# Performance work log

Hardware: AMD Instinct MI355X
Metric: run time of the kernel (lower is better)

## Reference

```python
import jax, jax.numpy as jnp
import numpy as np

B, T, F, H = 256, 128, 1024, 512  # batch, input_size (time window), feature_dim, hidden_size


def setup_inputs() -> dict:
    key = jax.random.key(0)
    ks = jax.random.split(key, 7)
    in1 = T + 2 * H
    return {
        "h": jax.random.normal(ks[0], (B, H), dtype=jnp.float32),
        "s": jax.random.normal(ks[1], (B, H), dtype=jnp.float32),
        "x": jax.random.normal(ks[2], (B, T, F), dtype=jnp.float32),
        "W1": jax.random.normal(ks[3], (T, in1), dtype=jnp.float32) / np.sqrt(in1),
        "b1": jnp.zeros((T,), dtype=jnp.float32),
        "W2": jax.random.normal(ks[4], (1, T), dtype=jnp.float32) / np.sqrt(T),
        "b2": jnp.zeros((1,), dtype=jnp.float32),
    }


def reference(h, s, x, W1, b1, W2, b2):
    feature_dim = x.shape[-1]
    xp = jnp.transpose(x, (2, 0, 1))                     # [F, B, T]
    hb = jnp.broadcast_to(h[None], (feature_dim,) + h.shape)  # [F, B, H]
    sb = jnp.broadcast_to(s[None], (feature_dim,) + s.shape)  # [F, B, H]
    cat = jnp.concatenate([xp, hb, sb], axis=-1)         # [F, B, T+2H]
    u = jnp.einsum('fbk,tk->fbt', cat, W1) + b1          # [F, B, T]
    e = jnp.einsum('fbt,ot->fbo', jnp.tanh(u), W2) + b2  # [F, B, 1]
    alpha = jax.nn.softmax(e, axis=0)[..., 0]            # softmax over feature dim -> [F, B]
    return alpha.T                                       # [B, F]
```

## Files before the change

kernel.cpp:

```cpp
#include <hip/hip_runtime.h>
#include <hip/hip_bf16.h>


#define B_N 256
#define T_N 128
#define F_N 1024
#define H_N 512
#define IN1 1152

typedef __bf16 bf16x8 __attribute__((ext_vector_type(8)));
typedef float f32x16 __attribute__((ext_vector_type(16)));
typedef float f32x4_t __attribute__((ext_vector_type(4)));

__device__ __forceinline__ float wave_reduce_sum(float v) {
#pragma unroll
  for (int off = 32; off >= 1; off >>= 1) v += __shfl_xor(v, off, 64);
  return v;
}
__device__ __forceinline__ float wave_reduce_max(float v) {
#pragma unroll
  for (int off = 32; off >= 1; off >>= 1) v = fmaxf(v, __shfl_xor(v, off, 64));
  return v;
}

__global__ __launch_bounds__(1024) void kA_c(const float* __restrict__ h,
                                             const float* __restrict__ s,
                                             const float* __restrict__ W1,
                                             const float* __restrict__ b1,
                                             float* __restrict__ c) {
  int tid = threadIdx.x;
  int lane = tid & 63, wid = tid >> 6;
  int tg = blockIdx.x >> 6;
  int bg = blockIdx.x & 63;
  int t = tg * 4 + (wid >> 2);
  int b = bg * 4 + (wid & 3);
  const float4* wrow = reinterpret_cast<const float4*>(W1 + t * IN1 + T_N);
  const float4* hrow = reinterpret_cast<const float4*>(h + b * H_N);
  const float4* srow = reinterpret_cast<const float4*>(s + b * H_N);
  float acc = 0.f;
#pragma unroll
  for (int i = 0; i < 4; ++i) {
    int j4 = i * 64 + lane;
    float4 w = wrow[j4];
    float4 v = (i < 2) ? hrow[j4] : srow[j4 - 128];
    acc += w.x * v.x + w.y * v.y + w.z * v.z + w.w * v.w;
  }
  acc = wave_reduce_sum(acc);
  if (lane == 0) c[b * T_N + t] = acc + b1[t];
}

__global__ __launch_bounds__(256) void kA_frag(const float* __restrict__ W1,
                                               unsigned short* __restrict__ w1frag) {
  int i = blockIdx.x * 256 + threadIdx.x;
  int p0 = i * 2;
  int j = p0 & 7;
  int lane = (p0 >> 3) & 63;
  int kk = (p0 >> 9) & 7;
  int tt = (p0 >> 12) & 3;
  int t = tt * 32 + (lane & 31);
  int k = kk * 16 + 8 * (lane >> 5) + j;
  const float2 w = *reinterpret_cast<const float2*>(W1 + t * IN1 + k);
  __bf16 a = (__bf16)w.x, bq = (__bf16)w.y;
  unsigned short ua = __builtin_bit_cast(unsigned short, a);
  unsigned short ub = __builtin_bit_cast(unsigned short, bq);
  *reinterpret_cast<unsigned*>(w1frag + p0) = (unsigned)ua | ((unsigned)ub << 16);
}

__global__ __launch_bounds__(256) void kB_e(const float* __restrict__ x,
                                            const unsigned short* __restrict__ w1frag,
                                            const float* __restrict__ c,
                                            const float* __restrict__ W2,
                                            const float* __restrict__ b2,
                                            float* __restrict__ e) {
  __shared__ __align__(16) unsigned short w1lds[16384];
  __shared__ __align__(16) float clds[T_N];
  __shared__ __align__(16) float w2lds[T_N];
  int tid = threadIdx.x;
  int b = blockIdx.x >> 3;
  int fg = blockIdx.x & 7;

  {
    const uint4* src = reinterpret_cast<const uint4*>(w1frag);
    uint4* dst = reinterpret_cast<uint4*>(w1lds);
#pragma unroll
    for (int i = 0; i < 8; ++i) dst[tid + 256 * i] = src[tid + 256 * i];
  }
  if (tid < T_N) clds[tid] = c[b * T_N + tid];
  else if (tid < 2 * T_N) w2lds[tid - T_N] = W2[tid - T_N];
  __syncthreads();

  int lane = tid & 63, wave = tid >> 6;
  int g = lane >> 5, l31 = lane & 31;
  int f0 = fg * 128 + wave * 32;

  const float* xb = x + (size_t)b * T_N * F_N + f0 + l31 + g * 8 * F_N;
  const bf16x8* af = reinterpret_cast<const bf16x8*>(w1lds);

  f32x16 acc0 = {}, acc1 = {}, acc2 = {}, acc3 = {};
#pragma unroll
  for (int kk = 0; kk < 8; ++kk) {
    float xv[8];
#pragma unroll
    for (int j = 0; j < 8; ++j) xv[j] = xb[(kk * 16 + j) * F_N];
    bf16x8 bfrag;
#pragma unroll
    for (int j = 0; j < 8; ++j) bfrag[j] = (__bf16)xv[j];
    int fidx = kk * 64 + lane;
    acc0 = __builtin_amdgcn_mfma_f32_32x32x16_bf16(af[fidx], bfrag, acc0, 0, 0, 0);
    acc1 = __builtin_amdgcn_mfma_f32_32x32x16_bf16(af[fidx + 512], bfrag, acc1, 0, 0, 0);
    acc2 = __builtin_amdgcn_mfma_f32_32x32x16_bf16(af[fidx + 1024], bfrag, acc2, 0, 0, 0);
    acc3 = __builtin_amdgcn_mfma_f32_32x32x16_bf16(af[fidx + 1536], bfrag, acc3, 0, 0, 0);
  }

  float esum = 0.f;
#define EPI(ACC, TT)                                                              \
  {                                                                               \
    int bt = TT * 32 + 4 * g;                                                     \
    _Pragma("unroll") for (int q = 0; q < 4; ++q) {                               \
      f32x4_t cq = *reinterpret_cast<const f32x4_t*>(&clds[bt + 8 * q]);          \
      f32x4_t wq = *reinterpret_cast<const f32x4_t*>(&w2lds[bt + 8 * q]);         \
      _Pragma("unroll") for (int r = 0; r < 4; ++r) {                             \
        float u = ACC[q * 4 + r] + cq[r];                                         \
        u = fminf(fmaxf(u, -15.f), 15.f);                                         \
        float e2 = __expf(2.f * u);                                               \
        float th = (e2 - 1.f) / (e2 + 1.f);                                       \
        esum += wq[r] * th;                                                       \
      }                                                                           \
    }                                                                             \
  }
  EPI(acc0, 0) EPI(acc1, 1) EPI(acc2, 2) EPI(acc3, 3)
#undef EPI

  esum += __shfl_xor(esum, 32, 64);
  if (g == 0) e[(size_t)b * F_N + f0 + l31] = esum + b2[0];
}

__global__ __launch_bounds__(256) void kC_softmax(float* __restrict__ out) {
  int b = blockIdx.x, tid = threadIdx.x;
  int lane = tid & 63, wid = tid >> 6;
  float* row = out + (size_t)b * F_N;
  float v[4];
#pragma unroll
  for (int q = 0; q < 4; ++q) v[q] = row[tid + 256 * q];
  float m = fmaxf(fmaxf(v[0], v[1]), fmaxf(v[2], v[3]));
  m = wave_reduce_max(m);
  __shared__ float rm[4], rs[4];
  if (lane == 0) rm[wid] = m;
  __syncthreads();
  float M = fmaxf(fmaxf(rm[0], rm[1]), fmaxf(rm[2], rm[3]));
  float ssum = 0.f;
#pragma unroll
  for (int q = 0; q < 4; ++q) {
    v[q] = __expf(v[q] - M);
    ssum += v[q];
  }
  ssum = wave_reduce_sum(ssum);
  if (lane == 0) rs[wid] = ssum;
  __syncthreads();
  float S = rs[0] + rs[1] + rs[2] + rs[3];
  float inv = 1.f / S;
#pragma unroll
  for (int q = 0; q < 4; ++q) row[tid + 256 * q] = v[q] * inv;
}

extern "C" void kernel_launch(void* const* d_in, const int* in_sizes, int n_in,
                              void* d_out, int out_size, void* d_ws, size_t ws_size,
                              hipStream_t stream) {
  const float* h = (const float*)d_in[0];
  const float* s = (const float*)d_in[1];
  const float* x = (const float*)d_in[2];
  const float* W1 = (const float*)d_in[3];
  const float* b1 = (const float*)d_in[4];
  const float* W2 = (const float*)d_in[5];
  const float* b2 = (const float*)d_in[6];
  float* out = (float*)d_out;

  float* c_ws = (float*)d_ws;
  unsigned short* w1frag = (unsigned short*)((char*)d_ws + B_N * T_N * 4);

  kA_c<<<2048, 1024, 0, stream>>>(h, s, W1, b1, c_ws);
  kA_frag<<<32, 256, 0, stream>>>(W1, w1frag);
  kB_e<<<2048, 256, 0, stream>>>(x, w1frag, c_ws, W2, b2, out);
  kC_softmax<<<256, 256, 0, stream>>>(out);
}
```

Before: 229.0 us.

## Restructure attention-score kernels for vectorized x loads and staged h/s reuse

```diff
diff --git a/kernel.cpp b/kernel.cpp
--- a/kernel.cpp
+++ b/kernel.cpp
@@ -23,30 +23,46 @@
   return v;
 }
 
-__global__ __launch_bounds__(1024) void kA_c(const float* __restrict__ h,
-                                             const float* __restrict__ s,
-                                             const float* __restrict__ W1,
-                                             const float* __restrict__ b1,
-                                             float* __restrict__ c) {
+__device__ __forceinline__ float tanh_fast(float u) {
+  u = fminf(fmaxf(u, -15.f), 15.f);
+  float e2 = __expf(2.f * u);
+  return (e2 - 1.f) / (e2 + 1.f);
+}
+
+#define HSP 1028
+__global__ __launch_bounds__(256) void kA_c(const float* __restrict__ h,
+                                            const float* __restrict__ s,
+                                            const float* __restrict__ W1,
+                                            const float* __restrict__ b1,
+                                            float* __restrict__ c) {
+  __shared__ __align__(16) float hs[8 * HSP];
   int tid = threadIdx.x;
-  int lane = tid & 63, wid = tid >> 6;
-  int tg = blockIdx.x >> 6;
-  int bg = blockIdx.x & 63;
-  int t = tg * 4 + (wid >> 2);
-  int b = bg * 4 + (wid & 3);
-  const float4* wrow = reinterpret_cast<const float4*>(W1 + t * IN1 + T_N);
-  const float4* hrow = reinterpret_cast<const float4*>(h + b * H_N);
-  const float4* srow = reinterpret_cast<const float4*>(s + b * H_N);
+  int bg = blockIdx.x >> 2;
+  int tg = blockIdx.x & 3;
+#pragma unroll
+  for (int i = 0; i < 8; ++i) {
+    int p = tid + 256 * i;
+    int bl = p >> 8;
+    int j4 = p & 255;
+    int b = bg * 8 + bl;
+    float4 v;
+    if (j4 < 128) v = reinterpret_cast<const float4*>(h + (size_t)b * H_N)[j4];
+    else v = reinterpret_cast<const float4*>(s + (size_t)b * H_N)[j4 - 128];
+    *reinterpret_cast<float4*>(&hs[bl * HSP + j4 * 4]) = v;
+  }
+  __syncthreads();
+  int bl = tid >> 5, ti = tid & 31;
+  int t = tg * 32 + ti;
+  int b = bg * 8 + bl;
+  const float4* wrow = reinterpret_cast<const float4*>(W1 + (size_t)t * IN1 + T_N);
+  const float4* vrow = reinterpret_cast<const float4*>(&hs[bl * HSP]);
   float acc = 0.f;
-#pragma unroll
-  for (int i = 0; i < 4; ++i) {
-    int j4 = i * 64 + lane;
-    float4 w = wrow[j4];
-    float4 v = (i < 2) ? hrow[j4] : srow[j4 - 128];
+#pragma unroll 4
+  for (int j4 = 0; j4 < 256; ++j4) {
+    float4 w = wrow[j4], v = vrow[j4];
     acc += w.x * v.x + w.y * v.y + w.z * v.z + w.w * v.w;
   }
-  acc = wave_reduce_sum(acc);
-  if (lane == 0) c[b * T_N + t] = acc + b1[t];
+  c[b * T_N + t] = acc + b1[t];
 }
 
 __global__ __launch_bounds__(256) void kA_frag(const float* __restrict__ W1,
@@ -75,6 +91,7 @@
   __shared__ __align__(16) unsigned short w1lds[16384];
   __shared__ __align__(16) float clds[T_N];
   __shared__ __align__(16) float w2lds[T_N];
+  __shared__ __align__(16) float epart[4][T_N];
   int tid = threadIdx.x;
   int b = blockIdx.x >> 3;
   int fg = blockIdx.x & 7;
@@ -91,48 +108,59 @@
 
   int lane = tid & 63, wave = tid >> 6;
   int g = lane >> 5, l31 = lane & 31;
-  int f0 = fg * 128 + wave * 32;
-
-  const float* xb = x + (size_t)b * T_N * F_N + f0 + l31 + g * 8 * F_N;
+  int f0 = fg * 128;
+
+  const float4* xb4 = reinterpret_cast<const float4*>(x + (size_t)b * T_N * F_N + f0);
   const bf16x8* af = reinterpret_cast<const bf16x8*>(w1lds);
 
   f32x16 acc0 = {}, acc1 = {}, acc2 = {}, acc3 = {};
 #pragma unroll
   for (int kk = 0; kk < 8; ++kk) {
-    float xv[8];
-#pragma unroll
-    for (int j = 0; j < 8; ++j) xv[j] = xb[(kk * 16 + j) * F_N];
-    bf16x8 bfrag;
-#pragma unroll
-    for (int j = 0; j < 8; ++j) bfrag[j] = (__bf16)xv[j];
-    int fidx = kk * 64 + lane;
-    acc0 = __builtin_amdgcn_mfma_f32_32x32x16_bf16(af[fidx], bfrag, acc0, 0, 0, 0);
-    acc1 = __builtin_amdgcn_mfma_f32_32x32x16_bf16(af[fidx + 512], bfrag, acc1, 0, 0, 0);
-    acc2 = __builtin_amdgcn_mfma_f32_32x32x16_bf16(af[fidx + 1024], bfrag, acc2, 0, 0, 0);
-    acc3 = __builtin_amdgcn_mfma_f32_32x32x16_bf16(af[fidx + 1536], bfrag, acc3, 0, 0, 0);
-  }
-
-  float esum = 0.f;
-#define EPI(ACC, TT)                                                              \
-  {                                                                               \
-    int bt = TT * 32 + 4 * g;                                                     \
-    _Pragma("unroll") for (int q = 0; q < 4; ++q) {                               \
-      f32x4_t cq = *reinterpret_cast<const f32x4_t*>(&clds[bt + 8 * q]);          \
-      f32x4_t wq = *reinterpret_cast<const f32x4_t*>(&w2lds[bt + 8 * q]);         \
-      _Pragma("unroll") for (int r = 0; r < 4; ++r) {                             \
-        float u = ACC[q * 4 + r] + cq[r];                                         \
-        u = fminf(fmaxf(u, -15.f), 15.f);                                         \
-        float e2 = __expf(2.f * u);                                               \
-        float th = (e2 - 1.f) / (e2 + 1.f);                                       \
-        esum += wq[r] * th;                                                       \
-      }                                                                           \
-    }                                                                             \
-  }
-  EPI(acc0, 0) EPI(acc1, 1) EPI(acc2, 2) EPI(acc3, 3)
-#undef EPI
-
-  esum += __shfl_xor(esum, 32, 64);
-  if (g == 0) e[(size_t)b * F_N + f0 + l31] = esum + b2[0];
+    float4 xq[8];
+#pragma unroll
+    for (int j = 0; j < 8; ++j)
+      xq[j] = xb4[(size_t)(kk * 16 + 8 * g + j) * 256 + l31];
+    bf16x8 bf0, bf1, bf2, bf3;
+#pragma unroll
+    for (int j = 0; j < 8; ++j) {
+      bf0[j] = (__bf16)xq[j].x;
+      bf1[j] = (__bf16)xq[j].y;
+      bf2[j] = (__bf16)xq[j].z;
+      bf3[j] = (__bf16)xq[j].w;
+    }
+    bf16x8 afr = af[wave * 512 + kk * 64 + lane];
+    acc0 = __builtin_amdgcn_mfma_f32_32x32x16_bf16(afr, bf0, acc0, 0, 0, 0);
+    acc1 = __builtin_amdgcn_mfma_f32_32x32x16_bf16(afr, bf1, acc1, 0, 0, 0);
+    acc2 = __builtin_amdgcn_mfma_f32_32x32x16_bf16(afr, bf2, acc2, 0, 0, 0);
+    acc3 = __builtin_amdgcn_mfma_f32_32x32x16_bf16(afr, bf3, acc3, 0, 0, 0);
+  }
+
+  int tbase = wave * 32 + 4 * g;
+  float4 es = {0.f, 0.f, 0.f, 0.f};
+#pragma unroll
+  for (int q = 0; q < 4; ++q) {
+    f32x4_t cq = *reinterpret_cast<const f32x4_t*>(&clds[tbase + 8 * q]);
+    f32x4_t wq = *reinterpret_cast<const f32x4_t*>(&w2lds[tbase + 8 * q]);
+#pragma unroll
+    for (int r = 0; r < 4; ++r) {
+      int reg = q * 4 + r;
+      float w2v = wq[r], cv = cq[r];
+      es.x += w2v * tanh_fast(acc0[reg] + cv);
+      es.y += w2v * tanh_fast(acc1[reg] + cv);
+      es.z += w2v * tanh_fast(acc2[reg] + cv);
+      es.w += w2v * tanh_fast(acc3[reg] + cv);
+    }
+  }
+  es.x += __shfl_xor(es.x, 32, 64);
+  es.y += __shfl_xor(es.y, 32, 64);
+  es.z += __shfl_xor(es.z, 32, 64);
+  es.w += __shfl_xor(es.w, 32, 64);
+  if (g == 0) *reinterpret_cast<float4*>(&epart[wave][4 * l31]) = es;
+  __syncthreads();
+  if (tid < T_N) {
+    float sum = epart[0][tid] + epart[1][tid] + epart[2][tid] + epart[3][tid] + b2[0];
+    e[(size_t)b * F_N + f0 + tid] = sum;
+  }
 }
 
 __global__ __launch_bounds__(256) void kC_softmax(float* __restrict__ out) {
@@ -178,7 +206,7 @@
   float* c_ws = (float*)d_ws;
   unsigned short* w1frag = (unsigned short*)((char*)d_ws + B_N * T_N * 4);
 
-  kA_c<<<2048, 1024, 0, stream>>>(h, s, W1, b1, c_ws);
+  kA_c<<<128, 256, 0, stream>>>(h, s, W1, b1, c_ws);
   kA_frag<<<32, 256, 0, stream>>>(W1, w1frag);
   kB_e<<<2048, 256, 0, stream>>>(x, w1frag, c_ws, W2, b2, out);
   kC_softmax<<<256, 256, 0, stream>>>(out);
```

New measurement: 250.4 us. 9.4% more time.
